# Kernel optimization log

Hardware: AMD Instinct MI355X
Metric: run time of the kernel (lower is better)

The kernel has to match this reference:

```python
import jax, jax.numpy as jnp
import numpy as np

B, N, CIN, H, E = 1, 20000, 128, 128, 320000


def setup_inputs() -> dict:
    key = jax.random.key(0)
    ks = jax.random.split(key, 16)
    x = jax.random.normal(ks[0], (B, N, CIN), jnp.float32)
    edge_index = jax.random.randint(ks[1], (2, E), 0, N, dtype=jnp.int64)
    edge_weight = jax.random.uniform(ks[2], (E,), jnp.float32)
    h = jax.random.normal(ks[3], (B, N, H), jnp.float32)
    c = jax.random.normal(ks[4], (B, N, H), jnp.float32)
    # GCN stack params, gate order [i, f, c, o]; 2 layers each (K=2)
    Wx0 = jax.random.normal(ks[5], (4, CIN, H), jnp.float32) / np.float32(np.sqrt(CIN))
    bx0 = jnp.zeros((4, H), jnp.float32)
    Wx1 = jax.random.normal(ks[6], (4, H, H), jnp.float32) / np.float32(np.sqrt(H))
    bx1 = jnp.zeros((4, H), jnp.float32)
    Wh0 = jax.random.normal(ks[7], (4, H, H), jnp.float32) / np.float32(np.sqrt(H))
    bh0 = jnp.zeros((4, H), jnp.float32)
    Wh1 = jax.random.normal(ks[8], (4, H, H), jnp.float32) / np.float32(np.sqrt(H))
    bh1 = jnp.zeros((4, H), jnp.float32)
    wc = jax.random.normal(ks[9], (3, H), jnp.float32) * 0.1  # peephole [i, f, o]
    bg = jnp.zeros((4, H), jnp.float32)  # gate biases [i, f, c, o]
    return dict(x=x, edge_index=edge_index, edge_weight=edge_weight, h=h, c=c,
                Wx0=Wx0, bx0=bx0, Wx1=Wx1, bx1=bx1,
                Wh0=Wh0, bh0=bh0, Wh1=Wh1, bh1=bh1, wc=wc, bg=bg)


def reference(x, edge_index, edge_weight, h, c,
              Wx0, bx0, Wx1, bx1, Wh0, bh0, Wh1, bh1, wc, bg):
    n = x.shape[1]
    src, dst = edge_index[0], edge_index[1]
    loop = jnp.arange(n)
    src2 = jnp.concatenate([src, loop])
    dst2 = jnp.concatenate([dst, loop])
    w2 = jnp.concatenate([edge_weight, jnp.ones((n,), edge_weight.dtype)])
    deg = jax.ops.segment_sum(w2, dst2, num_segments=n)
    dis = jnp.where(deg > 0, jax.lax.rsqrt(jnp.maximum(deg, 1e-12)), 0.0)
    norm = dis[src2] * w2 * dis[dst2]  # sym GCN norm with self loops

    def prop(t):  # t: [..., N, F] -> D^-1/2 (A+I) D^-1/2 t
        lead = t.shape[:-2]
        tf = t.reshape((-1,) + t.shape[-2:])
        m = tf[:, src2, :] * norm[None, :, None]
        agg = jax.vmap(lambda mm: jax.ops.segment_sum(mm, dst2, num_segments=n))(m)
        return agg.reshape(lead + agg.shape[-2:])

    def gcn4(t, W0, b0, W1, b1):  # 2-layer GCN, 4 gates at once
        a = prop(t)  # shared first aggregation: [B,N,F]
        h0 = jax.nn.relu(jnp.einsum('bnc,gch->gbnh', a, W0) + b0[:, None, None, :])
        a1 = prop(h0)  # [4,B,N,H]
        return jnp.einsum('gbnh,ghk->gbnk', a1, W1) + b1[:, None, None, :]

    G = gcn4(x, Wx0, bx0, Wx1, bx1) + gcn4(h, Wh0, bh0, Wh1, bh1)  # [4,B,N,H]
    I = jax.nn.sigmoid(G[0] + wc[0] * c + bg[0])
    F = jax.nn.sigmoid(G[1] + wc[1] * c + bg[1])
    T = jnp.tanh(G[2] + bg[2])
    Cn = F * c + I * T
    O = jax.nn.sigmoid(G[3] + wc[2] * Cn + bg[3])
    Hn = O * jnp.tanh(Cn)
    return (Hn, Cn)
```

## Files before the change

### kernel.cpp

```cpp
#include <hip/hip_runtime.h>
#include <hip/hip_bf16.h>
#include <stdint.h>

#define NN    20000
#define NP    20096
#define EE    320000
#define CH    128
#define GC    512
#define NHtot 2560000

typedef short bf16x8 __attribute__((ext_vector_type(8)));
typedef float f32x4  __attribute__((ext_vector_type(4)));

__device__ __forceinline__ float bf2f(unsigned short u) {
    union { unsigned int i; float f; } c; c.i = ((unsigned int)u) << 16; return c.f;
}
__device__ __forceinline__ unsigned short f2bf(float f) {
    __hip_bfloat16 b = __float2bfloat16(f);
    union { __hip_bfloat16 b; unsigned short u; } c; c.b = b; return c.u;
}
__device__ __forceinline__ void unpack8(uint4 v, float* f) {
    f[0] = bf2f((unsigned short)(v.x & 0xffff)); f[1] = bf2f((unsigned short)(v.x >> 16));
    f[2] = bf2f((unsigned short)(v.y & 0xffff)); f[3] = bf2f((unsigned short)(v.y >> 16));
    f[4] = bf2f((unsigned short)(v.z & 0xffff)); f[5] = bf2f((unsigned short)(v.z >> 16));
    f[6] = bf2f((unsigned short)(v.w & 0xffff)); f[7] = bf2f((unsigned short)(v.w >> 16));
}
__device__ __forceinline__ uint4 pack8(const float* f) {
    uint4 v;
    v.x = (unsigned int)f2bf(f[0]) | ((unsigned int)f2bf(f[1]) << 16);
    v.y = (unsigned int)f2bf(f[2]) | ((unsigned int)f2bf(f[3]) << 16);
    v.z = (unsigned int)f2bf(f[4]) | ((unsigned int)f2bf(f[5]) << 16);
    v.w = (unsigned int)f2bf(f[6]) | ((unsigned int)f2bf(f[7]) << 16);
    return v;
}
__device__ __forceinline__ void unpack4(uint2 v, float* f) {
    f[0] = bf2f((unsigned short)(v.x & 0xffff)); f[1] = bf2f((unsigned short)(v.x >> 16));
    f[2] = bf2f((unsigned short)(v.y & 0xffff)); f[3] = bf2f((unsigned short)(v.y >> 16));
}
__device__ __forceinline__ uint2 pack4(const float* f) {
    uint2 v;
    v.x = (unsigned int)f2bf(f[0]) | ((unsigned int)f2bf(f[1]) << 16);
    v.y = (unsigned int)f2bf(f[2]) | ((unsigned int)f2bf(f[3]) << 16);
    return v;
}

__global__ void k_count(const int* __restrict__ ei, const float* __restrict__ ew,
                        float* __restrict__ deg, int* __restrict__ cnt) {
    int e = blockIdx.x * 256 + threadIdx.x;
    if (e >= EE) return;
    int d = ei[EE + e];
    atomicAdd(&deg[d], ew[e]);
    atomicAdd(&cnt[d], 1);
}

__global__ void k_dis(float* __restrict__ deg) {
    int i = blockIdx.x * 256 + threadIdx.x;
    if (i >= NN) return;
    float dv = deg[i] + 1.0f;
    deg[i] = rsqrtf(fmaxf(dv, 1e-12f));
}

__global__ void k_scan1(const int* __restrict__ cnt, int* __restrict__ rowoff,
                        int* __restrict__ bsum) {
    __shared__ int wsum[4];
    int i = blockIdx.x * 256 + threadIdx.x;
    int self = (i < NN) ? cnt[i] : 0;
    int lane = threadIdx.x & 63, wid = threadIdx.x >> 6;
    int v = self;
    #pragma unroll
    for (int off = 1; off < 64; off <<= 1) {
        int u = __shfl_up(v, off);
        if (lane >= off) v += u;
    }
    if (lane == 63) wsum[wid] = v;
    __syncthreads();
    int wof = 0;
    for (int k = 0; k < wid; ++k) wof += wsum[k];
    if (i < NN) rowoff[i] = wof + v - self;
    if (threadIdx.x == 255) bsum[blockIdx.x] = wof + v;
}

__global__ void k_scan2(int* __restrict__ bsum) {
    int lane = threadIdx.x;
    int base = 0;
    for (int start = 0; start < 80; start += 64) {
        int i = start + lane;
        int self = (i < 80) ? bsum[i] : 0;
        int v = self;
        #pragma unroll
        for (int off = 1; off < 64; off <<= 1) {
            int u = __shfl_up(v, off);
            if (lane >= off) v += u;
        }
        if (i < 80) bsum[i] = base + v - self;
        base += __shfl(v, 63);
    }
}

__global__ void k_scan3(int* __restrict__ rowoff, const int* __restrict__ bsum,
                        int* __restrict__ cur) {
    int i = blockIdx.x * 256 + threadIdx.x;
    if (i < NN) {
        int v = rowoff[i] + bsum[i >> 8];
        rowoff[i] = v; cur[i] = v;
    }
    if (i == NN) rowoff[NN] = EE;
}

__global__ void k_scatter(const int* __restrict__ ei, const float* __restrict__ ew,
                          const float* __restrict__ dis, int* __restrict__ cur,
                          int* __restrict__ csrs, float* __restrict__ csrn) {
    int e = blockIdx.x * 256 + threadIdx.x;
    if (e >= EE) return;
    int s = ei[e], d = ei[EE + e];
    float nrm = dis[s] * ew[e] * dis[d];
    int p = atomicAdd(&cur[d], 1);
    csrs[p] = s; csrn[p] = nrm;
}

__global__ void k_castxh(const float* __restrict__ x, const float* __restrict__ h,
                         unsigned short* __restrict__ xhb) {
    int idx = blockIdx.x * 256 + threadIdx.x;
    int n = idx >> 5, c4 = idx & 31;
    float4 xv = *(const float4*)(x + (size_t)n * CH + c4 * 4);
    float4 hv = *(const float4*)(h + (size_t)n * CH + c4 * 4);
    float fx[4] = { xv.x, xv.y, xv.z, xv.w };
    float fh[4] = { hv.x, hv.y, hv.z, hv.w };
    *(uint2*)(xhb + (size_t)n * 256 + c4 * 4)       = pack4(fx);
    *(uint2*)(xhb + (size_t)n * 256 + 128 + c4 * 4) = pack4(fh);
}

__global__ __launch_bounds__(128) void k_prop256(
        const unsigned short* __restrict__ tab, unsigned short* __restrict__ o,
        const int* __restrict__ rowoff, const int* __restrict__ csrs,
        const float* __restrict__ csrn, const float* __restrict__ dis) {
    int w = blockIdx.x * 2 + (threadIdx.x >> 6);
    int lane = threadIdx.x & 63;
    const uint2* T2 = (const uint2*)tab;
    float dv = dis[w], sw = dv * dv;
    float acc[4], va[4], vb[4];
    uint2 v = T2[(size_t)w * 64 + lane];
    unpack4(v, va);
    #pragma unroll
    for (int j = 0; j < 4; ++j) acc[j] = sw * va[j];
    int e = rowoff[w], e1 = rowoff[w + 1];
    for (; e + 2 <= e1; e += 2) {
        int   s0 = csrs[e],     s1 = csrs[e + 1];
        float n0 = csrn[e],     n1 = csrn[e + 1];
        uint2 v0 = T2[(size_t)s0 * 64 + lane];
        uint2 v1 = T2[(size_t)s1 * 64 + lane];
        unpack4(v0, va); unpack4(v1, vb);
        #pragma unroll
        for (int j = 0; j < 4; ++j) acc[j] += n0 * va[j] + n1 * vb[j];
    }
    if (e < e1) {
        int s = csrs[e]; float nw = csrn[e];
        v = T2[(size_t)s * 64 + lane];
        unpack4(v, va);
        #pragma unroll
        for (int j = 0; j < 4; ++j) acc[j] += nw * va[j];
    }
    ((uint2*)o)[(size_t)w * 64 + lane] = pack4(acc);
}

__global__ void k_prepw(const float* __restrict__ W0, const float* __restrict__ W1,
                        const float* __restrict__ W2, const float* __restrict__ W3,
                        unsigned short* __restrict__ T0, unsigned short* __restrict__ T1,
                        unsigned short* __restrict__ T2, unsigned short* __restrict__ T3) {
    const float* W; unsigned short* T;
    switch (blockIdx.z) {
        case 0:  W = W0; T = T0; break;
        case 1:  W = W1; T = T1; break;
        case 2:  W = W2; T = T2; break;
        default: W = W3; T = T3; break;
    }
    int g = blockIdx.y;
    int n = blockIdx.x * 2 + (threadIdx.x >> 7);
    int k = threadIdx.x & 127;
    T[((size_t)g * 128 + n) * 128 + k] = f2bf(W[((size_t)g * 128 + k) * 128 + n]);
}

#define SWZ(r, c8) (((r) << 4) + ((c8) ^ ((r) & 15)))

__global__ __launch_bounds__(256) void k_gemm1(
        const unsigned short* __restrict__ A, int aoff,
        const unsigned short* __restrict__ Wt,
        const float* __restrict__ bias, unsigned short* __restrict__ out) {
    __shared__ uint4 As[2048];
    __shared__ uint4 Bs[2048];
    const int    g    = blockIdx.y;
    const size_t row0 = (size_t)blockIdx.x * 128;
    const int    t    = threadIdx.x;

    #pragma unroll
    for (int p = 0; p < 8; ++p) {
        int id = t + 256 * p, r = id >> 4, c8 = id & 15;
        As[SWZ(r, c8)] = *(const uint4*)(A + (row0 + r) * 256 + aoff + c8 * 8);
    }
    const unsigned short* Wg = Wt + (size_t)g * 16384;
    #pragma unroll
    for (int p = 0; p < 8; ++p) {
        int id = t + 256 * p, r = id >> 4, c8 = id & 15;
        Bs[SWZ(r, c8)] = *(const uint4*)(Wg + r * CH + c8 * 8);
    }
    __syncthreads();

    const int wid = t >> 6, l = t & 63;
    const int m0 = (wid >> 1) * 64, n0 = (wid & 1) * 64;
    const int lm = l & 15, q = l >> 4;
    f32x4 acc[4][4];
    #pragma unroll
    for (int i = 0; i < 4; ++i)
        #pragma unroll
        for (int j = 0; j < 4; ++j) { acc[i][j][0]=0.f; acc[i][j][1]=0.f; acc[i][j][2]=0.f; acc[i][j][3]=0.f; }

    #pragma unroll
    for (int kc = 0; kc < 4; ++kc) {
        int c8 = kc * 4 + q;
        bf16x8 a[4], b[4];
        #pragma unroll
        for (int i = 0; i < 4; ++i) { int r = m0 + i * 16 + lm; a[i] = *(const bf16x8*)&As[SWZ(r, c8)]; }
        #pragma unroll
        for (int j = 0; j < 4; ++j) { int r = n0 + j * 16 + lm; b[j] = *(const bf16x8*)&Bs[SWZ(r, c8)]; }
        #pragma unroll
        for (int i = 0; i < 4; ++i)
            #pragma unroll
            for (int j = 0; j < 4; ++j)
                acc[i][j] = __builtin_amdgcn_mfma_f32_16x16x32_bf16(a[i], b[j], acc[i][j], 0, 0, 0);
    }

    #pragma unroll
    for (int j = 0; j < 4; ++j) {
        float bb = bias[g * CH + n0 + j * 16 + lm];
        #pragma unroll
        for (int i = 0; i < 4; ++i)
            #pragma unroll
            for (int r = 0; r < 4; ++r) {
                int rowl = m0 + i * 16 + q * 4 + r;
                int col  = n0 + j * 16 + lm;
                out[(row0 + rowl) * GC + g * CH + col] = f2bf(fmaxf(acc[i][j][r] + bb, 0.f));
            }
    }
}

__global__ __launch_bounds__(256) void k_gemm2(
        const unsigned short* __restrict__ A1, const unsigned short* __restrict__ A2,
        const unsigned short* __restrict__ Wt1, const unsigned short* __restrict__ Wt2,
        unsigned short* __restrict__ outS) {
    __shared__ uint4 As[2048];
    __shared__ uint4 Bs[2048];
    const int    g    = blockIdx.y;
    const size_t row0 = (size_t)blockIdx.x * 128;
    const int    t    = threadIdx.x;
    const int wid = t >> 6, l = t & 63;
    const int m0 = (wid >> 1) * 64, n0 = (wid & 1) * 64;
    const int lm = l & 15, q = l >> 4;
    f32x4 acc[4][4];
    #pragma unroll
    for (int i = 0; i < 4; ++i)
        #pragma unroll
        for (int j = 0; j < 4; ++j) { acc[i][j][0]=0.f; acc[i][j][1]=0.f; acc[i][j][2]=0.f; acc[i][j][3]=0.f; }

    for (int side = 0; side < 2; ++side) {
        if (side) __syncthreads();
        const unsigned short* Ap = side ? A2 : A1;
        const unsigned short* Wg = (side ? Wt2 : Wt1) + (size_t)g * 16384;
        #pragma unroll
        for (int p = 0; p < 8; ++p) {
            int id = t + 256 * p, r = id >> 4, c8 = id & 15;
            As[SWZ(r, c8)] = *(const uint4*)(Ap + (row0 + r) * GC + g * CH + c8 * 8);
        }
        #pragma unroll
        for (int p = 0; p < 8; ++p) {
            int id = t + 256 * p, r = id >> 4, c8 = id & 15;
            Bs[SWZ(r, c8)] = *(const uint4*)(Wg + r * CH + c8 * 8);
        }
        __syncthreads();
        #pragma unroll
        for (int kc = 0; kc < 4; ++kc) {
            int c8 = kc * 4 + q;
            bf16x8 a[4], b[4];
            #pragma unroll
            for (int i = 0; i < 4; ++i) { int r = m0 + i * 16 + lm; a[i] = *(const bf16x8*)&As[SWZ(r, c8)]; }
            #pragma unroll
            for (int j = 0; j < 4; ++j) { int r = n0 + j * 16 + lm; b[j] = *(const bf16x8*)&Bs[SWZ(r, c8)]; }
            #pragma unroll
            for (int i = 0; i < 4; ++i)
                #pragma unroll
                for (int j = 0; j < 4; ++j)
                    acc[i][j] = __builtin_amdgcn_mfma_f32_16x16x32_bf16(a[i], b[j], acc[i][j], 0, 0, 0);
        }
    }

    #pragma unroll
    for (int j = 0; j < 4; ++j)
        #pragma unroll
        for (int i = 0; i < 4; ++i)
            #pragma unroll
            for (int r = 0; r < 4; ++r) {
                int rowl = m0 + i * 16 + q * 4 + r;
                int col  = n0 + j * 16 + lm;
                outS[(row0 + rowl) * GC + g * CH + col] = f2bf(acc[i][j][r]);
            }
}

__global__ __launch_bounds__(128) void k_prop512(
        const unsigned short* __restrict__ Sb, unsigned short* __restrict__ G0,
        const int* __restrict__ rowoff, const int* __restrict__ csrs,
        const float* __restrict__ csrn, const float* __restrict__ dis) {
    int w = blockIdx.x * 2 + (threadIdx.x >> 6);
    int lane = threadIdx.x & 63;
    const uint4* S4 = (const uint4*)Sb;
    float dv = dis[w], sw = dv * dv;
    float acc[8], va[8], vb[8];
    uint4 v = S4[(size_t)w * 64 + lane];
    unpack8(v, va);
    #pragma unroll
    for (int j = 0; j < 8; ++j) acc[j] = sw * va[j];
    int e = rowoff[w], e1 = rowoff[w + 1];
    for (; e + 2 <= e1; e += 2) {
        int   s0 = csrs[e],     s1 = csrs[e + 1];
        float n0 = csrn[e],     n1 = csrn[e + 1];
        uint4 v0 = S4[(size_t)s0 * 64 + lane];
        uint4 v1 = S4[(size_t)s1 * 64 + lane];
        unpack8(v0, va); unpack8(v1, vb);
        #pragma unroll
        for (int j = 0; j < 8; ++j) acc[j] += n0 * va[j] + n1 * vb[j];
    }
    if (e < e1) {
        int s = csrs[e]; float nw = csrn[e];
        v = S4[(size_t)s * 64 + lane];
        unpack8(v, va);
        #pragma unroll
        for (int j = 0; j < 8; ++j) acc[j] += nw * va[j];
    }
    ((uint4*)G0)[(size_t)w * 64 + lane] = pack8(acc);
}

__global__ void k_gates(const unsigned short* __restrict__ G0, const float* __restrict__ c,
                        const float* __restrict__ bx1, const float* __restrict__ bh1,
                        const float* __restrict__ wc, const float* __restrict__ bg,
                        float* __restrict__ out) {
    int idx = blockIdx.x * 256 + threadIdx.x;
    int n = idx >> 7, hh = idx & 127;
    size_t base = (size_t)n * GC + hh;
    float g0 = bf2f(G0[base])       + bx1[hh]       + bh1[hh];
    float g1 = bf2f(G0[base + 128]) + bx1[128 + hh] + bh1[128 + hh];
    float g2 = bf2f(G0[base + 256]) + bx1[256 + hh] + bh1[256 + hh];
    float g3 = bf2f(G0[base + 384]) + bx1[384 + hh] + bh1[384 + hh];
    float cv = c[idx];
    float I  = 1.f / (1.f + expf(-(g0 + wc[hh]       * cv + bg[hh])));
    float F  = 1.f / (1.f + expf(-(g1 + wc[128 + hh] * cv + bg[128 + hh])));
    float T  = tanhf(g2 + bg[256 + hh]);
    float Cn = F * cv + I * T;
    float O  = 1.f / (1.f + expf(-(g3 + wc[256 + hh] * Cn + bg[384 + hh])));
    out[idx]         = O * tanhf(Cn);
    out[NHtot + idx] = Cn;
}

extern "C" void kernel_launch(void* const* d_in, const int* in_sizes, int n_in,
                              void* d_out, int out_size, void* d_ws, size_t ws_size,
                              hipStream_t stream) {
    (void)in_sizes; (void)n_in; (void)out_size; (void)ws_size;
    const float* x   = (const float*)d_in[0];
    const int*   ei  = (const int*)d_in[1];
    const float* ew  = (const float*)d_in[2];
    const float* h   = (const float*)d_in[3];
    const float* c   = (const float*)d_in[4];
    const float* Wx0 = (const float*)d_in[5];
    const float* bx0 = (const float*)d_in[6];
    const float* Wx1 = (const float*)d_in[7];
    const float* bx1 = (const float*)d_in[8];
    const float* Wh0 = (const float*)d_in[9];
    const float* bh0 = (const float*)d_in[10];
    const float* Wh1 = (const float*)d_in[11];
    const float* bh1 = (const float*)d_in[12];
    const float* wc  = (const float*)d_in[13];
    const float* bg  = (const float*)d_in[14];
    float* out = (float*)d_out;

    float* wsf  = (float*)d_ws;
    float* deg  = wsf;
    int*   cnt  = (int*)(wsf + 20480);
    int*   row  = (int*)(wsf + 40960);
    int*   cur  = (int*)(wsf + 61696);
    int*   bsum = (int*)(wsf + 82176);
    int*   csrs = (int*)(wsf + 82432);
    float* csrn = wsf + 402432;
    unsigned short* Wt0x = (unsigned short*)(wsf + 722432);
    unsigned short* Wt0h = (unsigned short*)(wsf + 755200);
    unsigned short* Wt1x = (unsigned short*)(wsf + 787968);
    unsigned short* Wt1h = (unsigned short*)(wsf + 820736);
    unsigned short* xhb  = (unsigned short*)(wsf + 853504);
    unsigned short* axh  = (unsigned short*)(wsf + 3425792);
    unsigned short* h0x  = (unsigned short*)(wsf + 5998080);
    unsigned short* h0h  = (unsigned short*)(wsf + 11142656);
    unsigned short* Sb   = (unsigned short*)(wsf + 16287232);
    unsigned short* G0   = h0x;

    hipMemsetAsync(deg, 0, 2 * 20480 * sizeof(float), stream);

    k_count  <<<EE / 256, 256, 0, stream>>>(ei, ew, deg, cnt);
    k_dis    <<<(NN + 255) / 256, 256, 0, stream>>>(deg);
    k_scan1  <<<80, 256, 0, stream>>>(cnt, row, bsum);
    k_scan2  <<<1, 64, 0, stream>>>(bsum);
    k_scan3  <<<80, 256, 0, stream>>>(row, bsum, cur);
    k_scatter<<<EE / 256, 256, 0, stream>>>(ei, ew, deg, cur, csrs, csrn);

    dim3 pw(64, 4, 4);
    k_prepw  <<<pw, 256, 0, stream>>>(Wx0, Wh0, Wx1, Wh1, Wt0x, Wt0h, Wt1x, Wt1h);
    k_castxh <<<NN * 32 / 256, 256, 0, stream>>>(x, h, xhb);

    k_prop256<<<NN / 2, 128, 0, stream>>>(xhb, axh, row, csrs, csrn, deg);

    dim3 gg(NP / 128, 4);
    k_gemm1<<<gg, 256, 0, stream>>>(axh, 0,   Wt0x, bx0, h0x);
    k_gemm1<<<gg, 256, 0, stream>>>(axh, 128, Wt0h, bh0, h0h);
    k_gemm2<<<gg, 256, 0, stream>>>(h0x, h0h, Wt1x, Wt1h, Sb);

    k_prop512<<<NN / 2, 128, 0, stream>>>(Sb, G0, row, csrs, csrn, deg);
    k_gates  <<<NHtot / 256, 256, 0, stream>>>(G0, c, bx1, bh1, wc, bg, out);
}
```

Before: 287.8 us.

## Factor GCN normalization into node scaling, fuse gates into final propagation

The symmetric normalization is split into per-node D^-1/2 scaling applied before and after aggregation. This drops the per-edge normalized weights and the float atomic degree accumulation, which is replaced by a CSR row-sum kernel. The gate nonlinearity kernel is fused into the second propagation through shared memory, so the bf16 G0 round trip disappears. Biases are pre-summed, the two gemm1 launches are merged via blockIdx.z, and the gather loops are unrolled to 4 with 4 warps per block. Pre-scaling inputs in bf16 adds a little extra rounding.

```diff
diff --git a/kernel.cpp b/kernel.cpp
--- a/kernel.cpp
+++ b/kernel.cpp
@@ -25,14 +25,6 @@
     f[4] = bf2f((unsigned short)(v.z & 0xffff)); f[5] = bf2f((unsigned short)(v.z >> 16));
     f[6] = bf2f((unsigned short)(v.w & 0xffff)); f[7] = bf2f((unsigned short)(v.w >> 16));
 }
-__device__ __forceinline__ uint4 pack8(const float* f) {
-    uint4 v;
-    v.x = (unsigned int)f2bf(f[0]) | ((unsigned int)f2bf(f[1]) << 16);
-    v.y = (unsigned int)f2bf(f[2]) | ((unsigned int)f2bf(f[3]) << 16);
-    v.z = (unsigned int)f2bf(f[4]) | ((unsigned int)f2bf(f[5]) << 16);
-    v.w = (unsigned int)f2bf(f[6]) | ((unsigned int)f2bf(f[7]) << 16);
-    return v;
-}
 __device__ __forceinline__ void unpack4(uint2 v, float* f) {
     f[0] = bf2f((unsigned short)(v.x & 0xffff)); f[1] = bf2f((unsigned short)(v.x >> 16));
     f[2] = bf2f((unsigned short)(v.y & 0xffff)); f[3] = bf2f((unsigned short)(v.y >> 16));
@@ -44,20 +36,10 @@
     return v;
 }
 
-__global__ void k_count(const int* __restrict__ ei, const float* __restrict__ ew,
-                        float* __restrict__ deg, int* __restrict__ cnt) {
+__global__ void k_count(const int* __restrict__ ei, int* __restrict__ cnt) {
     int e = blockIdx.x * 256 + threadIdx.x;
     if (e >= EE) return;
-    int d = ei[EE + e];
-    atomicAdd(&deg[d], ew[e]);
-    atomicAdd(&cnt[d], 1);
-}
-
-__global__ void k_dis(float* __restrict__ deg) {
-    int i = blockIdx.x * 256 + threadIdx.x;
-    if (i >= NN) return;
-    float dv = deg[i] + 1.0f;
-    deg[i] = rsqrtf(fmaxf(dv, 1e-12f));
+    atomicAdd(&cnt[ei[EE + e]], 1);
 }
 
 __global__ void k_scan1(const int* __restrict__ cnt, int* __restrict__ rowoff,
@@ -108,58 +90,73 @@
 }
 
 __global__ void k_scatter(const int* __restrict__ ei, const float* __restrict__ ew,
-                          const float* __restrict__ dis, int* __restrict__ cur,
-                          int* __restrict__ csrs, float* __restrict__ csrn) {
+                          int* __restrict__ cur,
+                          int* __restrict__ csrs, float* __restrict__ csrw) {
     int e = blockIdx.x * 256 + threadIdx.x;
     if (e >= EE) return;
     int s = ei[e], d = ei[EE + e];
-    float nrm = dis[s] * ew[e] * dis[d];
     int p = atomicAdd(&cur[d], 1);
-    csrs[p] = s; csrn[p] = nrm;
+    csrs[p] = s; csrw[p] = ew[e];
+}
+
+__global__ void k_deg(const int* __restrict__ rowoff, const float* __restrict__ csrw,
+                      float* __restrict__ dis) {
+    int i = blockIdx.x * 256 + threadIdx.x;
+    if (i >= NN) return;
+    float s = 1.0f;
+    int e1 = rowoff[i + 1];
+    for (int e = rowoff[i]; e < e1; ++e) s += csrw[e];
+    dis[i] = rsqrtf(fmaxf(s, 1e-12f));
 }
 
 __global__ void k_castxh(const float* __restrict__ x, const float* __restrict__ h,
-                         unsigned short* __restrict__ xhb) {
+                         const float* __restrict__ dis, unsigned short* __restrict__ xhb) {
     int idx = blockIdx.x * 256 + threadIdx.x;
     int n = idx >> 5, c4 = idx & 31;
+    float dn = dis[n];
     float4 xv = *(const float4*)(x + (size_t)n * CH + c4 * 4);
     float4 hv = *(const float4*)(h + (size_t)n * CH + c4 * 4);
-    float fx[4] = { xv.x, xv.y, xv.z, xv.w };
-    float fh[4] = { hv.x, hv.y, hv.z, hv.w };
+    float fx[4] = { dn * xv.x, dn * xv.y, dn * xv.z, dn * xv.w };
+    float fh[4] = { dn * hv.x, dn * hv.y, dn * hv.z, dn * hv.w };
     *(uint2*)(xhb + (size_t)n * 256 + c4 * 4)       = pack4(fx);
     *(uint2*)(xhb + (size_t)n * 256 + 128 + c4 * 4) = pack4(fh);
 }
 
-__global__ __launch_bounds__(128) void k_prop256(
+__global__ __launch_bounds__(256) void k_prop256(
         const unsigned short* __restrict__ tab, unsigned short* __restrict__ o,
         const int* __restrict__ rowoff, const int* __restrict__ csrs,
-        const float* __restrict__ csrn, const float* __restrict__ dis) {
-    int w = blockIdx.x * 2 + (threadIdx.x >> 6);
+        const float* __restrict__ csrw, const float* __restrict__ dis) {
+    int w = blockIdx.x * 4 + (threadIdx.x >> 6);
     int lane = threadIdx.x & 63;
     const uint2* T2 = (const uint2*)tab;
-    float dv = dis[w], sw = dv * dv;
-    float acc[4], va[4], vb[4];
+    float acc[4], va[4], vb[4], vc[4], vd[4];
     uint2 v = T2[(size_t)w * 64 + lane];
     unpack4(v, va);
     #pragma unroll
-    for (int j = 0; j < 4; ++j) acc[j] = sw * va[j];
+    for (int j = 0; j < 4; ++j) acc[j] = va[j];
     int e = rowoff[w], e1 = rowoff[w + 1];
-    for (; e + 2 <= e1; e += 2) {
-        int   s0 = csrs[e],     s1 = csrs[e + 1];
-        float n0 = csrn[e],     n1 = csrn[e + 1];
-        uint2 v0 = T2[(size_t)s0 * 64 + lane];
-        uint2 v1 = T2[(size_t)s1 * 64 + lane];
-        unpack4(v0, va); unpack4(v1, vb);
-        #pragma unroll
-        for (int j = 0; j < 4; ++j) acc[j] += n0 * va[j] + n1 * vb[j];
-    }
-    if (e < e1) {
-        int s = csrs[e]; float nw = csrn[e];
+    for (; e + 4 <= e1; e += 4) {
+        int   s0 = csrs[e],   s1 = csrs[e+1], s2 = csrs[e+2], s3 = csrs[e+3];
+        float n0 = csrw[e],   n1 = csrw[e+1], n2 = csrw[e+2], n3 = csrw[e+3];
+        uint2 u0 = T2[(size_t)s0 * 64 + lane];
+        uint2 u1 = T2[(size_t)s1 * 64 + lane];
+        uint2 u2 = T2[(size_t)s2 * 64 + lane];
+        uint2 u3 = T2[(size_t)s3 * 64 + lane];
+        unpack4(u0, va); unpack4(u1, vb); unpack4(u2, vc); unpack4(u3, vd);
+        #pragma unroll
+        for (int j = 0; j < 4; ++j)
+            acc[j] += n0 * va[j] + n1 * vb[j] + n2 * vc[j] + n3 * vd[j];
+    }
+    for (; e < e1; ++e) {
+        int s = csrs[e]; float nw = csrw[e];
         v = T2[(size_t)s * 64 + lane];
         unpack4(v, va);
         #pragma unroll
         for (int j = 0; j < 4; ++j) acc[j] += nw * va[j];
     }
+    float dw = dis[w];
+    #pragma unroll
+    for (int j = 0; j < 4; ++j) acc[j] *= dw;
     ((uint2*)o)[(size_t)w * 64 + lane] = pack4(acc);
 }
 
@@ -180,14 +177,27 @@
     T[((size_t)g * 128 + n) * 128 + k] = f2bf(W[((size_t)g * 128 + k) * 128 + n]);
 }
 
+__global__ void k_prepb(const float* __restrict__ bx1, const float* __restrict__ bh1,
+                        const float* __restrict__ bg, float* __restrict__ btot) {
+    int f = blockIdx.x * 256 + threadIdx.x;
+    if (f < GC) btot[f] = bx1[f] + bh1[f] + bg[f];
+}
+
 #define SWZ(r, c8) (((r) << 4) + ((c8) ^ ((r) & 15)))
 
 __global__ __launch_bounds__(256) void k_gemm1(
-        const unsigned short* __restrict__ A, int aoff,
-        const unsigned short* __restrict__ Wt,
-        const float* __restrict__ bias, unsigned short* __restrict__ out) {
+        const unsigned short* __restrict__ A,
+        const unsigned short* __restrict__ Wtx, const unsigned short* __restrict__ Wth,
+        const float* __restrict__ bx0, const float* __restrict__ bh0,
+        unsigned short* __restrict__ outx, unsigned short* __restrict__ outh) {
     __shared__ uint4 As[2048];
     __shared__ uint4 Bs[2048];
+    const int side = blockIdx.z;
+    const int aoff = side * 128;
+    const unsigned short* Wt = side ? Wth : Wtx;
+    const float* bias        = side ? bh0 : bx0;
+    unsigned short* out      = side ? outh : outx;
+
     const int    g    = blockIdx.y;
     const size_t row0 = (size_t)blockIdx.x * 128;
     const int    t    = threadIdx.x;
@@ -246,7 +256,7 @@
 __global__ __launch_bounds__(256) void k_gemm2(
         const unsigned short* __restrict__ A1, const unsigned short* __restrict__ A2,
         const unsigned short* __restrict__ Wt1, const unsigned short* __restrict__ Wt2,
-        unsigned short* __restrict__ outS) {
+        const float* __restrict__ dis, unsigned short* __restrict__ outS) {
     __shared__ uint4 As[2048];
     __shared__ uint4 Bs[2048];
     const int    g    = blockIdx.y;
@@ -300,62 +310,69 @@
             for (int r = 0; r < 4; ++r) {
                 int rowl = m0 + i * 16 + q * 4 + r;
                 int col  = n0 + j * 16 + lm;
-                outS[(row0 + rowl) * GC + g * CH + col] = f2bf(acc[i][j][r]);
+                float dr = dis[row0 + rowl];
+                outS[(row0 + rowl) * GC + g * CH + col] = f2bf(dr * acc[i][j][r]);
             }
 }
 
-__global__ __launch_bounds__(128) void k_prop512(
-        const unsigned short* __restrict__ Sb, unsigned short* __restrict__ G0,
+#define GIDX(f) ((f) + ((f) >> 5))
+__global__ __launch_bounds__(256) void k_prop512g(
+        const unsigned short* __restrict__ Sb, float* __restrict__ out,
         const int* __restrict__ rowoff, const int* __restrict__ csrs,
-        const float* __restrict__ csrn, const float* __restrict__ dis) {
-    int w = blockIdx.x * 2 + (threadIdx.x >> 6);
-    int lane = threadIdx.x & 63;
+        const float* __restrict__ csrw, const float* __restrict__ dis,
+        const float* __restrict__ c, const float* __restrict__ btot,
+        const float* __restrict__ wc) {
+    __shared__ float gbuf[4][528];
+    int wid  = threadIdx.x >> 6, lane = threadIdx.x & 63;
+    int w    = blockIdx.x * 4 + wid;
     const uint4* S4 = (const uint4*)Sb;
-    float dv = dis[w], sw = dv * dv;
-    float acc[8], va[8], vb[8];
+    float acc[8], va[8], vb[8], vc4[8], vd[8];
     uint4 v = S4[(size_t)w * 64 + lane];
-    unpack8(v, va);
-    #pragma unroll
-    for (int j = 0; j < 8; ++j) acc[j] = sw * va[j];
+    unpack8(v, acc);
     int e = rowoff[w], e1 = rowoff[w + 1];
-    for (; e + 2 <= e1; e += 2) {
-        int   s0 = csrs[e],     s1 = csrs[e + 1];
-        float n0 = csrn[e],     n1 = csrn[e + 1];
-        uint4 v0 = S4[(size_t)s0 * 64 + lane];
-        uint4 v1 = S4[(size_t)s1 * 64 + lane];
-        unpack8(v0, va); unpack8(v1, vb);
-        #pragma unroll
-        for (int j = 0; j < 8; ++j) acc[j] += n0 * va[j] + n1 * vb[j];
-    }
-    if (e < e1) {
-        int s = csrs[e]; float nw = csrn[e];
+    for (; e + 4 <= e1; e += 4) {
+        int   s0 = csrs[e],   s1 = csrs[e+1], s2 = csrs[e+2], s3 = csrs[e+3];
+        float n0 = csrw[e],   n1 = csrw[e+1], n2 = csrw[e+2], n3 = csrw[e+3];
+        uint4 u0 = S4[(size_t)s0 * 64 + lane];
+        uint4 u1 = S4[(size_t)s1 * 64 + lane];
+        uint4 u2 = S4[(size_t)s2 * 64 + lane];
+        uint4 u3 = S4[(size_t)s3 * 64 + lane];
+        unpack8(u0, va); unpack8(u1, vb); unpack8(u2, vc4); unpack8(u3, vd);
+        #pragma unroll
+        for (int j = 0; j < 8; ++j)
+            acc[j] += n0 * va[j] + n1 * vb[j] + n2 * vc4[j] + n3 * vd[j];
+    }
+    for (; e < e1; ++e) {
+        int s = csrs[e]; float nw = csrw[e];
         v = S4[(size_t)s * 64 + lane];
         unpack8(v, va);
         #pragma unroll
         for (int j = 0; j < 8; ++j) acc[j] += nw * va[j];
     }
-    ((uint4*)G0)[(size_t)w * 64 + lane] = pack8(acc);
-}
-
-__global__ void k_gates(const unsigned short* __restrict__ G0, const float* __restrict__ c,
-                        const float* __restrict__ bx1, const float* __restrict__ bh1,
-                        const float* __restrict__ wc, const float* __restrict__ bg,
-                        float* __restrict__ out) {
-    int idx = blockIdx.x * 256 + threadIdx.x;
-    int n = idx >> 7, hh = idx & 127;
-    size_t base = (size_t)n * GC + hh;
-    float g0 = bf2f(G0[base])       + bx1[hh]       + bh1[hh];
-    float g1 = bf2f(G0[base + 128]) + bx1[128 + hh] + bh1[128 + hh];
-    float g2 = bf2f(G0[base + 256]) + bx1[256 + hh] + bh1[256 + hh];
-    float g3 = bf2f(G0[base + 384]) + bx1[384 + hh] + bh1[384 + hh];
-    float cv = c[idx];
-    float I  = 1.f / (1.f + expf(-(g0 + wc[hh]       * cv + bg[hh])));
-    float F  = 1.f / (1.f + expf(-(g1 + wc[128 + hh] * cv + bg[128 + hh])));
-    float T  = tanhf(g2 + bg[256 + hh]);
-    float Cn = F * cv + I * T;
-    float O  = 1.f / (1.f + expf(-(g3 + wc[256 + hh] * Cn + bg[384 + hh])));
-    out[idx]         = O * tanhf(Cn);
-    out[NHtot + idx] = Cn;
+    float dw = dis[w];
+    #pragma unroll
+    for (int j = 0; j < 8; ++j) {
+        int f = lane * 8 + j;
+        gbuf[wid][GIDX(f)] = dw * acc[j];
+    }
+    __syncthreads();
+    const float* gb = gbuf[wid];
+    #pragma unroll
+    for (int t2 = 0; t2 < 2; ++t2) {
+        int hh = lane + 64 * t2;
+        float g0 = gb[GIDX(hh)]       + btot[hh];
+        float g1 = gb[GIDX(128 + hh)] + btot[128 + hh];
+        float g2 = gb[GIDX(256 + hh)] + btot[256 + hh];
+        float g3 = gb[GIDX(384 + hh)] + btot[384 + hh];
+        float cv = c[(size_t)w * CH + hh];
+        float I  = 1.f / (1.f + expf(-(g0 + wc[hh]       * cv)));
+        float F  = 1.f / (1.f + expf(-(g1 + wc[128 + hh] * cv)));
+        float T  = tanhf(g2);
+        float Cn = F * cv + I * T;
+        float O  = 1.f / (1.f + expf(-(g3 + wc[256 + hh] * Cn)));
+        out[(size_t)w * CH + hh]         = O * tanhf(Cn);
+        out[NHtot + (size_t)w * CH + hh] = Cn;
+    }
 }
 
 extern "C" void kernel_launch(void* const* d_in, const int* in_sizes, int n_in,
@@ -380,44 +397,44 @@
     float* out = (float*)d_out;
 
     float* wsf  = (float*)d_ws;
-    float* deg  = wsf;
+    float* dis  = wsf;
     int*   cnt  = (int*)(wsf + 20480);
     int*   row  = (int*)(wsf + 40960);
     int*   cur  = (int*)(wsf + 61696);
     int*   bsum = (int*)(wsf + 82176);
-    int*   csrs = (int*)(wsf + 82432);
-    float* csrn = wsf + 402432;
-    unsigned short* Wt0x = (unsigned short*)(wsf + 722432);
-    unsigned short* Wt0h = (unsigned short*)(wsf + 755200);
-    unsigned short* Wt1x = (unsigned short*)(wsf + 787968);
-    unsigned short* Wt1h = (unsigned short*)(wsf + 820736);
-    unsigned short* xhb  = (unsigned short*)(wsf + 853504);
-    unsigned short* axh  = (unsigned short*)(wsf + 3425792);
-    unsigned short* h0x  = (unsigned short*)(wsf + 5998080);
-    unsigned short* h0h  = (unsigned short*)(wsf + 11142656);
-    unsigned short* Sb   = (unsigned short*)(wsf + 16287232);
-    unsigned short* G0   = h0x;
-
-    hipMemsetAsync(deg, 0, 2 * 20480 * sizeof(float), stream);
-
-    k_count  <<<EE / 256, 256, 0, stream>>>(ei, ew, deg, cnt);
-    k_dis    <<<(NN + 255) / 256, 256, 0, stream>>>(deg);
+    float* btot = wsf + 82432;
+    int*   csrs = (int*)(wsf + 82944);
+    float* csrw = wsf + 402944;
+    unsigned short* Wt0x = (unsigned short*)(wsf + 722944);
+    unsigned short* Wt0h = (unsigned short*)(wsf + 755712);
+    unsigned short* Wt1x = (unsigned short*)(wsf + 788480);
+    unsigned short* Wt1h = (unsigned short*)(wsf + 821248);
+    unsigned short* xhb  = (unsigned short*)(wsf + 854016);
+    unsigned short* axh  = (unsigned short*)(wsf + 3426304);
+    unsigned short* h0x  = (unsigned short*)(wsf + 5998592);
+    unsigned short* h0h  = (unsigned short*)(wsf + 11143168);
+    unsigned short* Sb   = (unsigned short*)(wsf + 16287744);
+
+    hipMemsetAsync(cnt, 0, 20480 * sizeof(int), stream);
+
+    k_count  <<<EE / 256, 256, 0, stream>>>(ei, cnt);
     k_scan1  <<<80, 256, 0, stream>>>(cnt, row, bsum);
     k_scan2  <<<1, 64, 0, stream>>>(bsum);
     k_scan3  <<<80, 256, 0, stream>>>(row, bsum, cur);
-    k_scatter<<<EE / 256, 256, 0, stream>>>(ei, ew, deg, cur, csrs, csrn);
+    k_scatter<<<EE / 256, 256, 0, stream>>>(ei, ew, cur, csrs, csrw);
+    k_deg    <<<(NN + 255) / 256, 256, 0, stream>>>(row, csrw, dis);
 
     dim3 pw(64, 4, 4);
     k_prepw  <<<pw, 256, 0, stream>>>(Wx0, Wh0, Wx1, Wh1, Wt0x, Wt0h, Wt1x, Wt1h);
-    k_castxh <<<NN * 32 / 256, 256, 0, stream>>>(x, h, xhb);
-
-    k_prop256<<<NN / 2, 128, 0, stream>>>(xhb, axh, row, csrs, csrn, deg);
-
-    dim3 gg(NP / 128, 4);
-    k_gemm1<<<gg, 256, 0, stream>>>(axh, 0,   Wt0x, bx0, h0x);
-    k_gemm1<<<gg, 256, 0, stream>>>(axh, 128, Wt0h, bh0, h0h);
-    k_gemm2<<<gg, 256, 0, stream>>>(h0x, h0h, Wt1x, Wt1h, Sb);
-
-    k_prop512<<<NN / 2, 128, 0, stream>>>(Sb, G0, row, csrs, csrn, deg);
-    k_gates  <<<NHtot / 256, 256, 0, stream>>>(G0, c, bx1, bh1, wc, bg, out);
-}
+    k_prepb  <<<2, 256, 0, stream>>>(bx1, bh1, bg, btot);
+    k_castxh <<<NN * 32 / 256, 256, 0, stream>>>(x, h, dis, xhb);
+
+    k_prop256<<<NN / 4, 256, 0, stream>>>(xhb, axh, row, csrs, csrw, dis);
+
+    dim3 g1(NP / 128, 4, 2);
+    k_gemm1<<<g1, 256, 0, stream>>>(axh, Wt0x, Wt0h, bx0, bh0, h0x, h0h);
+    dim3 g2(NP / 128, 4);
+    k_gemm2<<<g2, 256, 0, stream>>>(h0x, h0h, Wt1x, Wt1h, dis, Sb);
+
+    k_prop512g<<<NN / 4, 256, 0, stream>>>(Sb, out, row, csrs, csrw, dis, c, btot, wc);
+}
```

New measurement: 265.9 us. 1.08x faster.
